# Optimization experiments

Measured on AMD Instinct MI355X. Metric: run time of the kernel, lower is better.

The kernel has to match this reference:

```python
import jax, jax.numpy as jnp
import numpy as np

N_NODES = 100000
N_EDGES = 640000
IN_FEATS = 256
HEADS = 4
OUT_FEATS = 32
NEG_SLOPE = 0.2


def setup_inputs() -> dict:
    key = jax.random.key(0)
    k_feat, k_src, k_dst, k_w, k_al, k_ar = jax.random.split(key, 6)
    feat = jax.random.normal(k_feat, (N_NODES, IN_FEATS), dtype=jnp.float32)
    src = jax.random.randint(k_src, (N_EDGES,), 0, N_NODES, dtype=jnp.int32)
    dst = jax.random.randint(k_dst, (N_EDGES,), 0, N_NODES, dtype=jnp.int32)
    # fc: Linear(in_feats, out_feats*num_heads, bias=False); store as [in, H*D]
    W = jax.random.normal(k_w, (IN_FEATS, HEADS * OUT_FEATS), dtype=jnp.float32) * 0.05
    attn_l = jax.random.normal(k_al, (HEADS, OUT_FEATS), dtype=jnp.float32) * 0.1
    attn_r = jax.random.normal(k_ar, (HEADS, OUT_FEATS), dtype=jnp.float32) * 0.1
    return {"feat": feat, "W": W, "attn_l": attn_l, "attn_r": attn_r, "src": src, "dst": dst}


def reference(feat, W, attn_l, attn_r, src, dst):
    N = feat.shape[0]
    H, D = attn_l.shape
    # fc + reshape to [N, H, D]
    ft = (feat @ W).reshape(N, H, D)
    # per-node attention logits [N, H]
    el = jnp.einsum('nhd,hd->nh', ft, attn_l)
    er = jnp.einsum('nhd,hd->nh', ft, attn_r)
    # u_add_v then leaky relu -> per-edge logits [E, H]
    e = el[src] + er[dst]
    e = jnp.where(e > 0, e, NEG_SLOPE * e)
    # edge softmax over incoming edges of each dst node (per head)
    m = jax.ops.segment_max(e, dst, num_segments=N)  # [N, H]
    m = jnp.where(jnp.isfinite(m), m, jnp.zeros_like(m))  # empty segments
    ex = jnp.exp(e - m[dst])
    denom = jax.ops.segment_sum(ex, dst, num_segments=N)  # [N, H]
    a = ex / denom[dst]  # [E, H]
    # u_mul_e + sum aggregation: rst[v] = sum_{(u,v)} a_uv * ft[u]
    msg = ft[src] * a[:, :, None]  # [E, H, D]
    rst = jax.ops.segment_sum(msg, dst, num_segments=N)  # [N, H, D]
    return rst, a[:, :, None]
```

## Files before the change

kernel.cpp:

```cpp
#include <hip/hip_runtime.h>

#define N_NODES 100000
#define N_EDGES 640000
#define IN_F 256
#define HD 128

__global__ __launch_bounds__(256) void gemm_f32(const float* __restrict__ A,
    const float* __restrict__ B, float* __restrict__ C, int M)
{
  __shared__ float As[128][33];
  __shared__ float Bs[32][128];
  const int t = threadIdx.x;
  const int tx = t & 15, ty = t >> 4;
  const int rowBase = blockIdx.x * 128;
  float acc[8][8];
  #pragma unroll
  for (int i = 0; i < 8; i++)
    #pragma unroll
    for (int j = 0; j < 8; j++) acc[i][j] = 0.f;

  for (int k0 = 0; k0 < IN_F; k0 += 32) {
    #pragma unroll
    for (int i = 0; i < 4; i++) {
      int q = t + i * 256;
      int r = q >> 3, c4 = q & 7;
      int gr = rowBase + r; if (gr > M - 1) gr = M - 1;
      const float4 va = *(const float4*)(A + (size_t)gr * IN_F + k0 + c4 * 4);
      As[r][c4 * 4 + 0] = va.x; As[r][c4 * 4 + 1] = va.y;
      As[r][c4 * 4 + 2] = va.z; As[r][c4 * 4 + 3] = va.w;
    }
    #pragma unroll
    for (int i = 0; i < 4; i++) {
      int q = t + i * 256;
      int br = q >> 5, bc = q & 31;
      *(float4*)(&Bs[br][bc * 4]) = *(const float4*)(B + (size_t)(k0 + br) * HD + bc * 4);
    }
    __syncthreads();
    #pragma unroll
    for (int k = 0; k < 32; k++) {
      float av[8];
      #pragma unroll
      for (int i = 0; i < 8; i++) av[i] = As[ty * 8 + i][k];
      const float4 b0 = *(const float4*)(&Bs[k][tx * 4]);
      const float4 b1 = *(const float4*)(&Bs[k][64 + tx * 4]);
      #pragma unroll
      for (int i = 0; i < 8; i++) {
        acc[i][0] += av[i] * b0.x; acc[i][1] += av[i] * b0.y;
        acc[i][2] += av[i] * b0.z; acc[i][3] += av[i] * b0.w;
        acc[i][4] += av[i] * b1.x; acc[i][5] += av[i] * b1.y;
        acc[i][6] += av[i] * b1.z; acc[i][7] += av[i] * b1.w;
      }
    }
    __syncthreads();
  }
  #pragma unroll
  for (int i = 0; i < 8; i++) {
    int r = rowBase + ty * 8 + i;
    if (r < M) {
      float4 o0 = make_float4(acc[i][0], acc[i][1], acc[i][2], acc[i][3]);
      float4 o1 = make_float4(acc[i][4], acc[i][5], acc[i][6], acc[i][7]);
      *(float4*)(C + (size_t)r * HD + tx * 4) = o0;
      *(float4*)(C + (size_t)r * HD + 64 + tx * 4) = o1;
    }
  }
}

__global__ __launch_bounds__(256) void elr_kernel(const float* __restrict__ ft,
    const float* __restrict__ al, const float* __restrict__ ar,
    float* __restrict__ el, float* __restrict__ er, int n)
{
  int v = blockIdx.x * 4 + (threadIdx.x >> 6);
  if (v >= n) return;
  int lane = threadIdx.x & 63;
  float f0 = ft[(size_t)v * HD + lane], f1 = ft[(size_t)v * HD + 64 + lane];
  float l0 = f0 * al[lane],      l1 = f1 * al[64 + lane];
  float r0 = f0 * ar[lane],      r1 = f1 * ar[64 + lane];
  #pragma unroll
  for (int off = 16; off >= 1; off >>= 1) {
    l0 += __shfl_xor(l0, off); l1 += __shfl_xor(l1, off);
    r0 += __shfl_xor(r0, off); r1 += __shfl_xor(r1, off);
  }
  if ((lane & 31) == 0) {
    int g = lane >> 5;
    el[v * 4 + g] = l0; el[v * 4 + 2 + g] = l1;
    er[v * 4 + g] = r0; er[v * 4 + 2 + g] = r1;
  }
}

__global__ void deg_kernel(const int* __restrict__ dst, int* __restrict__ deg) {
  int i = blockIdx.x * blockDim.x + threadIdx.x;
  if (i < N_EDGES) atomicAdd(&deg[dst[i]], 1);
}

__global__ __launch_bounds__(256) void scanA(const int* __restrict__ deg,
    int* __restrict__ excl, int* __restrict__ partials, int n)
{
  __shared__ int s[256];
  int t = threadIdx.x;
  int base = blockIdx.x * 1024 + t * 4;
  int d0 = (base + 0 < n) ? deg[base + 0] : 0;
  int d1 = (base + 1 < n) ? deg[base + 1] : 0;
  int d2 = (base + 2 < n) ? deg[base + 2] : 0;
  int d3 = (base + 3 < n) ? deg[base + 3] : 0;
  int sum = d0 + d1 + d2 + d3;
  s[t] = sum; __syncthreads();
  for (int off = 1; off < 256; off <<= 1) {
    int x = 0; if (t >= off) x = s[t - off];
    __syncthreads(); s[t] += x; __syncthreads();
  }
  int e0 = s[t] - sum;
  if (base + 0 < n) excl[base + 0] = e0;
  if (base + 1 < n) excl[base + 1] = e0 + d0;
  if (base + 2 < n) excl[base + 2] = e0 + d0 + d1;
  if (base + 3 < n) excl[base + 3] = e0 + d0 + d1 + d2;
  if (t == 255) partials[blockIdx.x] = s[255];
}

__global__ void scanB(int* partials, int nb) {
  __shared__ int s[128];
  int t = threadIdx.x;
  int v = (t < nb) ? partials[t] : 0;
  s[t] = v; __syncthreads();
  for (int off = 1; off < 128; off <<= 1) {
    int x = 0; if (t >= off) x = s[t - off];
    __syncthreads(); s[t] += x; __syncthreads();
  }
  if (t < nb) partials[t] = s[t] - v;
}

__global__ __launch_bounds__(256) void scanC(int* __restrict__ row_ptr,
    const int* __restrict__ partials, int n, int E)
{
  int t = threadIdx.x;
  int base = blockIdx.x * 1024 + t * 4;
  int add = partials[blockIdx.x];
  #pragma unroll
  for (int j = 0; j < 4; j++) if (base + j < n) row_ptr[base + j] += add;
  if (blockIdx.x == 0 && t == 0) row_ptr[n] = E;
}

__global__ void scatter_kernel(const int* __restrict__ src, const int* __restrict__ dst,
                               const int* __restrict__ row_ptr,
                               int* __restrict__ cursor, int* __restrict__ usrc) {
  int e = blockIdx.x * blockDim.x + threadIdx.x;
  if (e >= N_EDGES) return;
  int d = dst[e];
  int pos = row_ptr[d] + atomicAdd(&cursor[d], 1);
  usrc[pos] = src[e];
}

__global__ __launch_bounds__(256) void gat_node(const int* __restrict__ row_ptr,
    const int* __restrict__ usrc,
    const float* __restrict__ el, const float* __restrict__ er4,
    const float* __restrict__ ft, float* __restrict__ rst,
    float* __restrict__ lse, int n)
{
  __shared__ int   su[4][64];
  __shared__ float sex[4][64][4];
  const int w = threadIdx.x >> 6;
  const int lane = threadIdx.x & 63;
  const int v = blockIdx.x * 4 + w;
  if (v >= n) return;
  const int s0 = row_ptr[v];
  const int d  = row_ptr[v + 1] - s0;
  const int g  = lane >> 4;

  if (d == 0) {
    *(float2*)(rst + (size_t)v * HD + 2 * lane) = make_float2(0.f, 0.f);
    return;
  }

  const float4 erv = *(const float4*)(er4 + (size_t)v * 4);
  float m0 = -1e30f, m1 = -1e30f, m2 = -1e30f, m3 = -1e30f;
  float den = 0.f;
  float2 acc = make_float2(0.f, 0.f);

  for (int c0 = 0; c0 < d; c0 += 64) {
    const int cd = min(64, d - c0);
    float x0 = -1e30f, x1 = -1e30f, x2 = -1e30f, x3 = -1e30f;
    int u = 0;
    if (lane < cd) {
      u = usrc[s0 + c0 + lane];
      const float4 elv = *(const float4*)(el + (size_t)u * 4);
      x0 = elv.x + erv.x; x0 = x0 > 0.f ? x0 : 0.2f * x0;
      x1 = elv.y + erv.y; x1 = x1 > 0.f ? x1 : 0.2f * x1;
      x2 = elv.z + erv.z; x2 = x2 > 0.f ? x2 : 0.2f * x2;
      x3 = elv.w + erv.w; x3 = x3 > 0.f ? x3 : 0.2f * x3;
    }
    su[w][lane] = u;
    float n0 = x0, n1 = x1, n2 = x2, n3 = x3;
    #pragma unroll
    for (int off = 32; off >= 1; off >>= 1) {
      n0 = fmaxf(n0, __shfl_xor(n0, off));
      n1 = fmaxf(n1, __shfl_xor(n1, off));
      n2 = fmaxf(n2, __shfl_xor(n2, off));
      n3 = fmaxf(n3, __shfl_xor(n3, off));
    }
    n0 = fmaxf(n0, m0); n1 = fmaxf(n1, m1); n2 = fmaxf(n2, m2); n3 = fmaxf(n3, m3);
    float e0 = __expf(x0 - n0), e1 = __expf(x1 - n1);
    float e2 = __expf(x2 - n2), e3 = __expf(x3 - n3);
    sex[w][lane][0] = e0; sex[w][lane][1] = e1;
    sex[w][lane][2] = e2; sex[w][lane][3] = e3;
    float mg = g == 0 ? m0 : g == 1 ? m1 : g == 2 ? m2 : m3;
    float ng = g == 0 ? n0 : g == 1 ? n1 : g == 2 ? n2 : n3;
    float scale = __expf(mg - ng);
    den *= scale; acc.x *= scale; acc.y *= scale;
    m0 = n0; m1 = n1; m2 = n2; m3 = n3;
    asm volatile("s_waitcnt lgkmcnt(0)" ::: "memory");
    #pragma unroll 4
    for (int j = 0; j < cd; ++j) {
      int uu = su[w][j];
      float wgt = sex[w][j][g];
      float2 f = *(const float2*)(ft + (size_t)uu * HD + 2 * lane);
      den += wgt;
      acc.x += wgt * f.x; acc.y += wgt * f.y;
    }
  }
  *(float2*)(rst + (size_t)v * HD + 2 * lane) = make_float2(acc.x / den, acc.y / den);
  if ((lane & 15) == 0) {
    float mg = g == 0 ? m0 : g == 1 ? m1 : g == 2 ? m2 : m3;
    lse[(size_t)v * 4 + g] = mg + __logf(den);
  }
}

__global__ void norm_kernel(const int* __restrict__ src, const int* __restrict__ dst,
                            const float* __restrict__ el, const float* __restrict__ er,
                            const float* __restrict__ lse, float* __restrict__ a, int E)
{
  int i = blockIdx.x * blockDim.x + threadIdx.x;
  if (i >= E) return;
  int u = src[i], v = dst[i];
  const float4 elv = *(const float4*)(el + (size_t)u * 4);
  const float4 erv = *(const float4*)(er + (size_t)v * 4);
  const float4 ls  = *(const float4*)(lse + (size_t)v * 4);
  float x0 = elv.x + erv.x; x0 = x0 > 0.f ? x0 : 0.2f * x0;
  float x1 = elv.y + erv.y; x1 = x1 > 0.f ? x1 : 0.2f * x1;
  float x2 = elv.z + erv.z; x2 = x2 > 0.f ? x2 : 0.2f * x2;
  float x3 = elv.w + erv.w; x3 = x3 > 0.f ? x3 : 0.2f * x3;
  float4 o;
  o.x = __expf(x0 - ls.x); o.y = __expf(x1 - ls.y);
  o.z = __expf(x2 - ls.z); o.w = __expf(x3 - ls.w);
  *(float4*)(a + (size_t)i * 4) = o;
}

extern "C" void kernel_launch(void* const* d_in, const int* in_sizes, int n_in,
                              void* d_out, int out_size, void* d_ws, size_t ws_size,
                              hipStream_t stream)
{
  const float* feat = (const float*)d_in[0];
  const float* W    = (const float*)d_in[1];
  const float* al   = (const float*)d_in[2];
  const float* ar   = (const float*)d_in[3];
  const int*   src  = (const int*)d_in[4];
  const int*   dst  = (const int*)d_in[5];
  float* rst   = (float*)d_out;
  float* a_out = rst + (size_t)N_NODES * HD;

  char* w = (char*)d_ws;
  auto alloc = [&](size_t bytes) { char* p = w; w += (bytes + 255) & ~(size_t)255; return p; };
  float* ft      = (float*)alloc((size_t)N_NODES * HD * 4);
  float* el      = (float*)alloc((size_t)N_NODES * 4 * 4);
  float* er      = (float*)alloc((size_t)N_NODES * 4 * 4);
  float* lse     = (float*)alloc((size_t)N_NODES * 4 * 4);
  int*   deg     = (int*)alloc((size_t)N_NODES * 4);
  int*   row_ptr = (int*)alloc(((size_t)N_NODES + 1) * 4);
  int*   cursor  = (int*)alloc((size_t)N_NODES * 4);
  int*   partials= (int*)alloc(1024);
  int*   usrc    = (int*)alloc((size_t)N_EDGES * 4);

  hipMemsetAsync(deg, 0, N_NODES * 4, stream);
  hipMemsetAsync(cursor, 0, N_NODES * 4, stream);

  gemm_f32<<<(N_NODES + 127) / 128, 256, 0, stream>>>(feat, W, ft, N_NODES);
  elr_kernel<<<(N_NODES + 3) / 4, 256, 0, stream>>>(ft, al, ar, el, er, N_NODES);
  deg_kernel<<<(N_EDGES + 255) / 256, 256, 0, stream>>>(dst, deg);
  scanA<<<98, 256, 0, stream>>>(deg, row_ptr, partials, N_NODES);
  scanB<<<1, 128, 0, stream>>>(partials, 98);
  scanC<<<98, 256, 0, stream>>>(row_ptr, partials, N_NODES, N_EDGES);
  scatter_kernel<<<(N_EDGES + 255) / 256, 256, 0, stream>>>(src, dst, row_ptr, cursor, usrc);
  gat_node<<<(N_NODES + 3) / 4, 256, 0, stream>>>(row_ptr, usrc, el, er, ft, rst, lse, N_NODES);
  norm_kernel<<<(N_EDGES + 255) / 256, 256, 0, stream>>>(src, dst, el, er, lse, a_out, N_EDGES);
}
```

Measured before the change: 404.3 us.

## Replace FP32 SIMT GEMM with split-bf16 MFMA GEMM

Replaces the shared-memory FP32 FMA GEMM with a matrix-core kernel using 16x16x32 bf16 MFMA instructions. Each fp32 value is split into high and low bf16 parts, and three MFMAs per tile approximate fp32 accuracy. A small prep kernel converts and transposes W into bf16 hi/lo buffers. Operands now load straight from global memory with no LDS staging, and output stores are scalar, which may cost memory efficiency. Precision is slightly lower than true fp32.

```diff
diff --git a/kernel.cpp b/kernel.cpp
--- a/kernel.cpp
+++ b/kernel.cpp
@@ -5,62 +5,103 @@
 #define IN_F 256
 #define HD 128
 
-__global__ __launch_bounds__(256) void gemm_f32(const float* __restrict__ A,
-    const float* __restrict__ B, float* __restrict__ C, int M)
-{
-  __shared__ float As[128][33];
-  __shared__ float Bs[32][128];
-  const int t = threadIdx.x;
-  const int tx = t & 15, ty = t >> 4;
-  const int rowBase = blockIdx.x * 128;
-  float acc[8][8];
-  #pragma unroll
-  for (int i = 0; i < 8; i++)
-    #pragma unroll
-    for (int j = 0; j < 8; j++) acc[i][j] = 0.f;
-
-  for (int k0 = 0; k0 < IN_F; k0 += 32) {
-    #pragma unroll
-    for (int i = 0; i < 4; i++) {
-      int q = t + i * 256;
-      int r = q >> 3, c4 = q & 7;
-      int gr = rowBase + r; if (gr > M - 1) gr = M - 1;
-      const float4 va = *(const float4*)(A + (size_t)gr * IN_F + k0 + c4 * 4);
-      As[r][c4 * 4 + 0] = va.x; As[r][c4 * 4 + 1] = va.y;
-      As[r][c4 * 4 + 2] = va.z; As[r][c4 * 4 + 3] = va.w;
-    }
-    #pragma unroll
-    for (int i = 0; i < 4; i++) {
-      int q = t + i * 256;
-      int br = q >> 5, bc = q & 31;
-      *(float4*)(&Bs[br][bc * 4]) = *(const float4*)(B + (size_t)(k0 + br) * HD + bc * 4);
-    }
-    __syncthreads();
-    #pragma unroll
-    for (int k = 0; k < 32; k++) {
-      float av[8];
+using f32x4 = __attribute__((ext_vector_type(4))) float;
+using s8v   = __attribute__((ext_vector_type(8))) short;
+
+__device__ __forceinline__ unsigned short bf16rn(float x) {
+  unsigned u = __builtin_bit_cast(unsigned, x);
+  return (unsigned short)((u + 0x7FFFu + ((u >> 16) & 1u)) >> 16);
+}
+__device__ __forceinline__ float bf16tof(unsigned short h) {
+  unsigned u = ((unsigned)h) << 16;
+  return __builtin_bit_cast(float, u);
+}
+
+__global__ __launch_bounds__(256) void prep_b(const float* __restrict__ W,
+    short* __restrict__ Bth, short* __restrict__ Btl)
+{
+  int t = threadIdx.x;
+  int c = t >> 1;
+  int kbase = (t & 1) * 128;
+  #pragma unroll 8
+  for (int kk = 0; kk < 128; ++kk) {
+    int k = kbase + kk;
+    float w = W[(size_t)k * HD + c];
+    unsigned short h = bf16rn(w);
+    unsigned short l = bf16rn(w - bf16tof(h));
+    Bth[(size_t)c * IN_F + k] = (short)h;
+    Btl[(size_t)c * IN_F + k] = (short)l;
+  }
+}
+
+__global__ __launch_bounds__(256) void gemm_mfma(const float* __restrict__ feat,
+    const short* __restrict__ Bth, const short* __restrict__ Btl,
+    float* __restrict__ ft, int M)
+{
+  const int wid  = threadIdx.x >> 6;
+  const int lane = threadIdx.x & 63;
+  const int lr = lane & 15;
+  const int lg = lane >> 4;
+  const int wm = (wid >> 1) * 64;
+  const int wn = (wid & 1) * 64;
+  const int rb = blockIdx.x * 128;
+
+  f32x4 acc[4][4];
+  #pragma unroll
+  for (int i = 0; i < 4; i++)
+    #pragma unroll
+    for (int j = 0; j < 4; j++) acc[i][j] = (f32x4){0.f, 0.f, 0.f, 0.f};
+
+  int rowg[4];
+  #pragma unroll
+  for (int mi = 0; mi < 4; mi++) {
+    int r = rb + wm + mi * 16 + lr;
+    rowg[mi] = r < M ? r : M - 1;
+  }
+
+  #pragma unroll
+  for (int kt = 0; kt < 8; ++kt) {
+    const int k0 = kt * 32;
+    s8v bh[4], bl[4];
+    #pragma unroll
+    for (int ni = 0; ni < 4; ni++) {
+      int c = wn + ni * 16 + lr;
+      bh[ni] = *(const s8v*)(Bth + (size_t)c * IN_F + k0 + lg * 8);
+      bl[ni] = *(const s8v*)(Btl + (size_t)c * IN_F + k0 + lg * 8);
+    }
+    #pragma unroll
+    for (int mi = 0; mi < 4; mi++) {
+      const float* ap = feat + (size_t)rowg[mi] * IN_F + k0 + lg * 8;
+      const float4 a0 = *(const float4*)ap;
+      const float4 a1 = *(const float4*)(ap + 4);
+      float av[8] = {a0.x, a0.y, a0.z, a0.w, a1.x, a1.y, a1.z, a1.w};
+      s8v ah, al;
       #pragma unroll
-      for (int i = 0; i < 8; i++) av[i] = As[ty * 8 + i][k];
-      const float4 b0 = *(const float4*)(&Bs[k][tx * 4]);
-      const float4 b1 = *(const float4*)(&Bs[k][64 + tx * 4]);
+      for (int j = 0; j < 8; j++) {
+        unsigned short h = bf16rn(av[j]);
+        ah[j] = (short)h;
+        al[j] = (short)bf16rn(av[j] - bf16tof(h));
+      }
       #pragma unroll
-      for (int i = 0; i < 8; i++) {
-        acc[i][0] += av[i] * b0.x; acc[i][1] += av[i] * b0.y;
-        acc[i][2] += av[i] * b0.z; acc[i][3] += av[i] * b0.w;
-        acc[i][4] += av[i] * b1.x; acc[i][5] += av[i] * b1.y;
-        acc[i][6] += av[i] * b1.z; acc[i][7] += av[i] * b1.w;
+      for (int ni = 0; ni < 4; ni++) {
+        acc[mi][ni] = __builtin_amdgcn_mfma_f32_16x16x32_bf16(ah, bh[ni], acc[mi][ni], 0, 0, 0);
+        acc[mi][ni] = __builtin_amdgcn_mfma_f32_16x16x32_bf16(ah, bl[ni], acc[mi][ni], 0, 0, 0);
+        acc[mi][ni] = __builtin_amdgcn_mfma_f32_16x16x32_bf16(al, bh[ni], acc[mi][ni], 0, 0, 0);
       }
     }
-    __syncthreads();
-  }
-  #pragma unroll
-  for (int i = 0; i < 8; i++) {
-    int r = rowBase + ty * 8 + i;
-    if (r < M) {
-      float4 o0 = make_float4(acc[i][0], acc[i][1], acc[i][2], acc[i][3]);
-      float4 o1 = make_float4(acc[i][4], acc[i][5], acc[i][6], acc[i][7]);
-      *(float4*)(C + (size_t)r * HD + tx * 4) = o0;
-      *(float4*)(C + (size_t)r * HD + 64 + tx * 4) = o1;
+  }
+
+  #pragma unroll
+  for (int mi = 0; mi < 4; mi++) {
+    int rbase = rb + wm + mi * 16 + lg * 4;
+    #pragma unroll
+    for (int ni = 0; ni < 4; ni++) {
+      int col = wn + ni * 16 + lr;
+      #pragma unroll
+      for (int r = 0; r < 4; r++) {
+        int grow = rbase + r;
+        if (grow < M) ft[(size_t)grow * HD + col] = acc[mi][ni][r];
+      }
     }
   }
 }
@@ -267,11 +308,14 @@
   int*   cursor  = (int*)alloc((size_t)N_NODES * 4);
   int*   partials= (int*)alloc(1024);
   int*   usrc    = (int*)alloc((size_t)N_EDGES * 4);
+  short* Bth     = (short*)alloc((size_t)HD * IN_F * 2);
+  short* Btl     = (short*)alloc((size_t)HD * IN_F * 2);
 
   hipMemsetAsync(deg, 0, N_NODES * 4, stream);
   hipMemsetAsync(cursor, 0, N_NODES * 4, stream);
 
-  gemm_f32<<<(N_NODES + 127) / 128, 256, 0, stream>>>(feat, W, ft, N_NODES);
+  prep_b<<<1, 256, 0, stream>>>(W, Bth, Btl);
+  gemm_mfma<<<(N_NODES + 127) / 128, 256, 0, stream>>>(feat, Bth, Btl, ft, N_NODES);
   elr_kernel<<<(N_NODES + 3) / 4, 256, 0, stream>>>(ft, al, ar, el, er, N_NODES);
   deg_kernel<<<(N_EDGES + 255) / 256, 256, 0, stream>>>(dst, deg);
   scanA<<<98, 256, 0, stream>>>(deg, row_ptr, partials, N_NODES);
```

New measurement: 427.6 us. 1.06x slower.
